# Performance work log

Hardware: AMD Instinct MI355X
Metric: run time of the kernel (lower is better)

Reference implementation:

```python
import jax, jax.numpy as jnp
from jax import lax
import numpy as np

C = 12        # input channels
H = 233       # lstm hidden
L = 6         # lstm layers
P = 96        # sliding window length
F = 96        # forecast steps
B = 16        # batch (treated as SEQ axis by the LSTM, matching the torch code)


def setup_inputs() -> dict:
    key = jax.random.key(0)
    ks = jax.random.split(key, 9)
    s = 1.0 / np.sqrt(H)  # pytorch default uniform init scale
    u = lambda k, shape: jax.random.uniform(k, shape, jnp.float32, -s, s)
    return {
        "X": jax.random.normal(ks[0], (B, P, C), jnp.float32),
        "Wih0": u(ks[1], (4 * H, C)),        # layer 0 input weights
        "Wih": u(ks[2], (L - 1, 4 * H, H)),  # layers 1..5 input weights
        "Whh": u(ks[3], (L, 4 * H, H)),
        "bih": u(ks[4], (L, 4 * H)),
        "bhh": u(ks[5], (L, 4 * H)),
        "Wl": u(ks[6], (C, H)),
        "bl": u(ks[7], (C,)),
    }


def _lstm_layer(x, wih, whh, b):
    # x: (S, N, in) -> (S, N, H); scan over seq axis 0, gate order i,f,g,o (pytorch)
    N = x.shape[1]
    h0 = jnp.zeros((N, H), x.dtype)

    def cell(carry, xt):
        h, c = carry
        gates = xt @ wih.T + h @ whh.T + b          # (N, 4H)
        i, f, g, o = jnp.split(gates, 4, axis=-1)
        c = jax.nn.sigmoid(f) * c + jax.nn.sigmoid(i) * jnp.tanh(g)
        h = jax.nn.sigmoid(o) * jnp.tanh(c)
        return (h, c), h

    _, ys = lax.scan(cell, (h0, h0), x)
    return ys


def reference(X, Wih0, Wih, Whh, bih, bhh, Wl, bl):
    # Faithful to torch: nn.LSTM without batch_first treats axis0=B as seq,
    # axis1=P as batch; output[0][:, -1, :] picks the last window position.
    def step(window, _):
        x = _lstm_layer(window, Wih0, Whh[0], bih[0] + bhh[0])
        for l in range(1, L):
            x = _lstm_layer(x, Wih[l - 1], Whh[l], bih[l] + bhh[l])
        h_last = x[:, -1, :]              # (B, H)
        new = h_last @ Wl.T + bl          # (B, C)
        window = jnp.concatenate([window[:, 1:, :], new[:, None, :]], axis=1)
        return window, new

    _, toks = lax.scan(step, X, None, length=F)   # (F, B, C)
    return jnp.transpose(toks, (1, 0, 2))          # (B, F, C)
```

## Files before the change

### kernel.cpp

```cpp
#include <hip/hip_runtime.h>

#define HND    233
#define NL     6
#define GPL    8
#define UPW    32
#define ROWS   128
#define TSTEPS 16
#define FSTEPS 96
#define NSLOT  (TSTEPS*FSTEPS)
#define CDIM   12
#define G4H    (4*HND)
#define HP     240
#define VINW   496
#define NTICK  (6*95+15+1)
#define NHEAD  3
#define BLOCK  512
#define NWORD  234
#define AG     __HIP_MEMORY_SCOPE_AGENT
#define SENT   0x7FBADBADu
#define PLIM   (1L << 18)

typedef unsigned long long u64;

__device__ __forceinline__ float sigf(float x) { return 1.f / (1.f + expf(-x)); }
__device__ __forceinline__ bool rdy(u64 v) {
  return ((unsigned)v != SENT) && ((unsigned)(v >> 32) != SENT);
}

__device__ __forceinline__ int build(int m, int* fl, int* tl) {
  const int fh0 = m / 6;
  const int f_hi = (fh0 > 95) ? 95 : fh0;
  const int f_lo = (m < 10) ? 0 : (m - 10) / 6;
  const int ns = f_hi - f_lo + 1;
  #pragma unroll
  for (int k = 0; k < 3; ++k) { fl[k] = f_lo + k; tl[k] = m - 6 * (f_lo + k); }
  return ns;
}

__global__ void init_kernel(unsigned* __restrict__ hout, int hp) {
  size_t i = (size_t)blockIdx.x * blockDim.x + threadIdx.x;
  size_t stride = (size_t)gridDim.x * blockDim.x;
  const size_t nh = (size_t)NL * NSLOT * hp;
  for (size_t k = i; k < nh; k += stride) hout[k] = ((int)(k % hp) < HND) ? SENT : 0u;
}

__global__ void __launch_bounds__(BLOCK, 1) lstm_pipe(
    const float* __restrict__ X,
    const float* __restrict__ Wih0, const float* __restrict__ Wih,
    const float* __restrict__ Whh,  const float* __restrict__ bih,
    const float* __restrict__ bhh,  const float* __restrict__ Wl,
    const float* __restrict__ bl,   float* __restrict__ out,
    float* __restrict__ hout, int hps) {
  __shared__ float vin[3][VINW];
  __shared__ float bias[ROWS];
  __shared__ float foldb[ROWS];
  __shared__ float cst[3][UPW];
  __shared__ float wih0s[ROWS][CDIM];
  __shared__ float xs[TSTEPS][CDIM];
  __shared__ float wlh[CDIM][HP];

  const int tid = threadIdx.x;
  const int bid = blockIdx.x;
  u64* hu = (u64*)hout;

  if (bid >= NL * GPL) {
    const int hid = bid - NL * GPL;
    for (int i = tid; i < CDIM * HP; i += BLOCK) {
      int rr = i / HP, k = i % HP;
      ((float*)wlh)[i] = (k < HND) ? Wl[rr * HND + k] : 0.f;
    }
    for (int i = tid; i < VINW; i += BLOCK) vin[0][i] = 0.f;
    __syncthreads();
    for (int f = hid; f < FSTEPS; f += NHEAD) {
      for (int t = 0; t < TSTEPS; ++t) {
        if (tid < 117) {
          const u64* src = hu + ((size_t)5 * NSLOT + 16 * f + t) * hps + tid;
          u64 v; long gd = 0;
          for (;;) {
            v = __hip_atomic_load(src, __ATOMIC_RELAXED, AG);
            if (rdy(v)) break;
            if (++gd > PLIM) break;
            if (gd > 4) __builtin_amdgcn_s_sleep(1);
          }
          *(u64*)&vin[0][2 * tid] = v;
        }
        __syncthreads();
        if (tid < 48) {
          int rr = tid >> 2, q = tid & 3;
          const float4* wr = (const float4*)&wlh[rr][0];
          const float4* hv = (const float4*)&vin[0][0];
          float a = 0.f;
          #pragma unroll
          for (int c = 0; c < 15; ++c) {
            float4 x0 = wr[q * 15 + c], y0 = hv[q * 15 + c];
            a = fmaf(x0.w, y0.w, fmaf(x0.z, y0.z, fmaf(x0.y, y0.y, fmaf(x0.x, y0.x, a))));
          }
          a += __shfl_xor(a, 1);
          a += __shfl_xor(a, 2);
          if (q == 0) out[((size_t)t * FSTEPS + f) * CDIM + rr] = a + bl[rr];
        }
        __syncthreads();
      }
    }
    return;
  }

  const int l = bid / GPL, g = bid % GPL;
  const int j0 = g * UPW;
  const int U = min(UPW, HND - j0);
  const int wave = tid >> 6, ln = tid & 63;
  const int rr = ln & 15, q = ln >> 4;
  const int row = wave * 16 + rr;
  const int u = row >> 2, gt = row & 3;
  const int grow = gt * HND + j0 + u;
  const bool rowok = (u < U);

  if (l == 0) {
    for (int i = tid; i < CDIM * HP; i += BLOCK) {
      int r2 = i / HP, k = i % HP;
      ((float*)wlh)[i] = (k < HND) ? Wl[r2 * HND + k] : 0.f;
    }
    for (int i = tid; i < ROWS * CDIM; i += BLOCK) {
      int r2 = i / CDIM, c = i % CDIM;
      int uu = r2 >> 2, g2 = r2 & 3;
      wih0s[r2][c] = (uu < U) ? Wih0[(g2 * HND + j0 + uu) * CDIM + c] : 0.f;
    }
    for (int i = tid; i < TSTEPS * CDIM; i += BLOCK)
      xs[i / CDIM][i % CDIM] = X[((size_t)(i / CDIM) * 96 + 95) * CDIM + (i % CDIM)];
  }
  for (int i = tid; i < 3 * VINW; i += BLOCK) ((float*)vin)[i] = 0.f;
  __syncthreads();

  float4 w4[30];
  const float* wihl = Wih + (size_t)(l - 1) * G4H * HND;
  const float* whhl = Whh + (size_t)l * G4H * HND;
  #pragma unroll
  for (int j = 0; j < 30; ++j) {
    float e[4];
    #pragma unroll
    for (int ee = 0; ee < 4; ++ee) {
      const int idx = (q * 30 + j) * 4 + ee;
      float v = 0.f;
      if (rowok) {
        if (idx < HND) {
          if (l == 0) {
            float acc = 0.f;
            #pragma unroll
            for (int c = 0; c < CDIM; ++c) acc = fmaf(wih0s[row][c], wlh[c][idx], acc);
            v = acc;
          } else {
            v = wihl[(size_t)grow * HND + idx];
          }
        } else if (idx >= HP && idx < HP + HND) {
          v = whhl[(size_t)grow * HND + (idx - HP)];
        }
      }
      e[ee] = v;
    }
    w4[j] = make_float4(e[0], e[1], e[2], e[3]);
  }
  if (tid < ROWS) {
    float b = 0.f, fb = 0.f;
    if ((tid >> 2) < U) {
      const int gr2 = (tid & 3) * HND + j0 + (tid >> 2);
      b = bih[l * G4H + gr2] + bhh[l * G4H + gr2];
      if (l == 0) {
        #pragma unroll
        for (int c = 0; c < CDIM; ++c) fb = fmaf(wih0s[tid][c], bl[c], fb);
      }
    }
    bias[tid] = b;
    foldb[tid] = fb;
  }
  __syncthreads();

  int fl[3], tl[3];

  for (int m = 0; m < NTICK; ++m) {
    const int ns = build(m, fl, tl);

    const u64 *s0 = nullptr, *s1 = nullptr;
    u64 *d0 = nullptr, *d1 = nullptr;

    auto setup = [&](int w, const u64*& sp, u64*& dp) {
      const int k = w / NWORD;
      if (k >= ns) return;
      const int f = fl[k], t = tl[k], sg = f % 3;
      const int o = w - k * NWORD;
      if (o < 117) {
        if (l == 0 && f == 0) return;
        sp = (l == 0)
           ? hu + ((size_t)5 * NSLOT + 16 * (f - 1) + t) * hps + o
           : hu + ((size_t)(l - 1) * NSLOT + 16 * f + t) * hps + o;
        dp = (u64*)&vin[sg][2 * o];
      } else {
        const int jj = o - 117;
        float* dst = &vin[sg][HP + 2 * jj];
        if (t == 0) { dst[0] = 0.f; dst[1] = 0.f; return; }
        if ((jj >> 4) == g) return;
        sp = hu + ((size_t)l * NSLOT + 16 * f + (t - 1)) * hps + jj;
        dp = (u64*)dst;
      }
    };
    setup(tid, s0, d0);
    if (tid + BLOCK < 3 * NWORD) setup(tid + BLOCK, s1, d1);

    long gd = 0;
    while (s0 || s1) {
      if (s0) { u64 v = __hip_atomic_load(s0, __ATOMIC_RELAXED, AG);
                if (rdy(v)) { *d0 = v; s0 = nullptr; } }
      if (s1) { u64 v = __hip_atomic_load(s1, __ATOMIC_RELAXED, AG);
                if (rdy(v)) { *d1 = v; s1 = nullptr; } }
      if (++gd > PLIM) break;
      if (gd > 6) __builtin_amdgcn_s_sleep(1);
    }
    __syncthreads();

    float r0 = 0.f, r1 = 0.f, r2 = 0.f;
    {
      const float4* va = (const float4*)&vin[fl[0] % 3][0];
      float a = 0.f;
      #pragma unroll
      for (int j = 0; j < 30; ++j) {
        const float4 wv = w4[j];
        const float4 y = va[q * 30 + j];
        a = fmaf(wv.x, y.x, fmaf(wv.y, y.y, fmaf(wv.z, y.z, fmaf(wv.w, y.w, a))));
      }
      a += __shfl_xor(a, 16);
      a += __shfl_xor(a, 32);
      r0 = a + bias[row];
    }
    if (ns > 1) {
      const float4* vb = (const float4*)&vin[fl[1] % 3][0];
      float a = 0.f;
      #pragma unroll
      for (int j = 0; j < 30; ++j) {
        const float4 wv = w4[j];
        const float4 y = vb[q * 30 + j];
        a = fmaf(wv.x, y.x, fmaf(wv.y, y.y, fmaf(wv.z, y.z, fmaf(wv.w, y.w, a))));
      }
      a += __shfl_xor(a, 16);
      a += __shfl_xor(a, 32);
      r1 = a + bias[row];
    }
    if (ns > 2) {
      const float4* vc = (const float4*)&vin[fl[2] % 3][0];
      float a = 0.f;
      #pragma unroll
      for (int j = 0; j < 30; ++j) {
        const float4 wv = w4[j];
        const float4 y = vc[q * 30 + j];
        a = fmaf(wv.x, y.x, fmaf(wv.y, y.y, fmaf(wv.z, y.z, fmaf(wv.w, y.w, a))));
      }
      a += __shfl_xor(a, 16);
      a += __shfl_xor(a, 32);
      r2 = a + bias[row];
    }
    __syncthreads();

    const int v4 = ln & 3;
    const int uu = 4 * wave + v4;
    const int rowc = 4 * uu;
    #pragma unroll
    for (int k = 0; k < 3; ++k) {
      if (k >= ns) break;
      const int f = fl[k], t = tl[k], b3 = f % 3;
      const float gv = (k == 0) ? r0 : (k == 1) ? r1 : r2;
      float hn = 0.f;
      float gg[4];
      #pragma unroll
      for (int g2 = 0; g2 < 4; ++g2) gg[g2] = __shfl(gv, 4 * v4 + g2);
      if (ln < 4 && uu < U) {
        #pragma unroll
        for (int g2 = 0; g2 < 4; ++g2) {
          if (l == 0) {
            if (f == 0) {
              float s = gg[g2];
              #pragma unroll
              for (int c = 0; c < CDIM; ++c) s = fmaf(wih0s[rowc + g2][c], xs[t][c], s);
              gg[g2] = s;
            } else {
              gg[g2] += foldb[rowc + g2];
            }
          }
        }
        const float cp = (t == 0) ? 0.f : cst[b3][uu];
        const float cn = sigf(gg[1]) * cp + sigf(gg[0]) * tanhf(gg[2]);
        hn = sigf(gg[3]) * tanhf(cn);
        cst[b3][uu] = cn;
        vin[b3][HP + j0 + uu] = hn;
      }
      const float lo = __shfl(hn, 2 * (ln & 1));
      const float hi = __shfl(hn, 2 * (ln & 1) + 1);
      if (ln < 2) {
        const int pairu = 4 * wave + 2 * ln;
        if (pairu < U) {
          const u64 pv = ((u64)__float_as_uint(hi) << 32) | (u64)__float_as_uint(lo);
          __hip_atomic_store(hu + ((size_t)l * NSLOT + 16 * f + t) * hps +
                                 (j0 >> 1) + (pairu >> 1),
                             pv, __ATOMIC_RELAXED, AG);
        }
      }
    }
  }
}

extern "C" void kernel_launch(void* const* d_in, const int* in_sizes, int n_in,
                              void* d_out, int out_size, void* d_ws, size_t ws_size,
                              hipStream_t stream) {
  const float* X    = (const float*)d_in[0];
  const float* Wih0 = (const float*)d_in[1];
  const float* Wih  = (const float*)d_in[2];
  const float* Whh  = (const float*)d_in[3];
  const float* bih  = (const float*)d_in[4];
  const float* bhh  = (const float*)d_in[5];
  const float* Wl   = (const float*)d_in[6];
  const float* bl   = (const float*)d_in[7];

  const size_t HN = (size_t)NL * NSLOT;
  const int hp = (ws_size >= HN * 240 * 4) ? 240 : 234;
  float* hout = (float*)d_ws;

  init_kernel<<<2048, 256, 0, stream>>>((unsigned*)hout, hp);
  lstm_pipe<<<NL * GPL + NHEAD, BLOCK, 0, stream>>>(
      X, Wih0, Wih, Whh, bih, bhh, Wl, bl, (float*)d_out, hout, hp / 2);
}
```

Measured before the change: 2.762 ms.

## Spread LSTM units over more blocks and double-buffer per-tick input vectors

Each layer now spans 15 blocks of 256 threads, 16 units each, instead of 8 blocks of 512 threads with 32 units. The per-tick input vectors are double-buffered by tick parity and slot index, which removes the second barrier between the matvec and the cell update. Cell state moves from shared memory into registers. The three matvecs are fused into one loop that reuses each weight load. This spreads the serial recurrent work over more CUs, but more blocks now poll the flags and more cross-block traffic is needed per tick.

```diff
diff --git a/kernel.cpp b/kernel.cpp
--- a/kernel.cpp
+++ b/kernel.cpp
@@ -2,19 +2,19 @@
 
 #define HND    233
 #define NL     6
-#define GPL    8
-#define UPW    32
-#define ROWS   128
+#define GPL    15
+#define UPW    16
+#define ROWS   64
 #define TSTEPS 16
 #define FSTEPS 96
 #define NSLOT  (TSTEPS*FSTEPS)
 #define CDIM   12
 #define G4H    (4*HND)
 #define HP     240
-#define VINW   496
+#define RL     480
 #define NTICK  (6*95+15+1)
 #define NHEAD  3
-#define BLOCK  512
+#define BLOCK  256
 #define NWORD  234
 #define AG     __HIP_MEMORY_SCOPE_AGENT
 #define SENT   0x7FBADBADu
@@ -31,10 +31,9 @@
   const int fh0 = m / 6;
   const int f_hi = (fh0 > 95) ? 95 : fh0;
   const int f_lo = (m < 10) ? 0 : (m - 10) / 6;
-  const int ns = f_hi - f_lo + 1;
   #pragma unroll
   for (int k = 0; k < 3; ++k) { fl[k] = f_lo + k; tl[k] = m - 6 * (f_lo + k); }
-  return ns;
+  return f_hi - f_lo + 1;
 }
 
 __global__ void init_kernel(unsigned* __restrict__ hout, int hp) {
@@ -51,10 +50,9 @@
     const float* __restrict__ bhh,  const float* __restrict__ Wl,
     const float* __restrict__ bl,   float* __restrict__ out,
     float* __restrict__ hout, int hps) {
-  __shared__ float vin[3][VINW];
+  __shared__ float vin[2][3][RL];
   __shared__ float bias[ROWS];
   __shared__ float foldb[ROWS];
-  __shared__ float cst[3][UPW];
   __shared__ float wih0s[ROWS][CDIM];
   __shared__ float xs[TSTEPS][CDIM];
   __shared__ float wlh[CDIM][HP];
@@ -69,7 +67,7 @@
       int rr = i / HP, k = i % HP;
       ((float*)wlh)[i] = (k < HND) ? Wl[rr * HND + k] : 0.f;
     }
-    for (int i = tid; i < VINW; i += BLOCK) vin[0][i] = 0.f;
+    for (int i = tid; i < RL; i += BLOCK) vin[0][0][i] = 0.f;
     __syncthreads();
     for (int f = hid; f < FSTEPS; f += NHEAD) {
       for (int t = 0; t < TSTEPS; ++t) {
@@ -82,13 +80,13 @@
             if (++gd > PLIM) break;
             if (gd > 4) __builtin_amdgcn_s_sleep(1);
           }
-          *(u64*)&vin[0][2 * tid] = v;
+          *(u64*)&vin[0][0][2 * tid] = v;
         }
         __syncthreads();
         if (tid < 48) {
           int rr = tid >> 2, q = tid & 3;
           const float4* wr = (const float4*)&wlh[rr][0];
-          const float4* hv = (const float4*)&vin[0][0];
+          const float4* hv = (const float4*)&vin[0][0][0];
           float a = 0.f;
           #pragma unroll
           for (int c = 0; c < 15; ++c) {
@@ -128,7 +126,7 @@
     for (int i = tid; i < TSTEPS * CDIM; i += BLOCK)
       xs[i / CDIM][i % CDIM] = X[((size_t)(i / CDIM) * 96 + 95) * CDIM + (i % CDIM)];
   }
-  for (int i = tid; i < 3 * VINW; i += BLOCK) ((float*)vin)[i] = 0.f;
+  for (int i = tid; i < 2 * 3 * RL; i += BLOCK) ((float*)vin)[i] = 0.f;
   __syncthreads();
 
   float4 w4[30];
@@ -174,132 +172,118 @@
   }
   __syncthreads();
 
+  float cs0 = 0.f, cs1 = 0.f, cs2 = 0.f;
+  const int v4 = ln & 3;
+  const int ug = j0 + 4 * wave + v4;
   int fl[3], tl[3];
 
   for (int m = 0; m < NTICK; ++m) {
     const int ns = build(m, fl, tl);
-
-    const u64 *s0 = nullptr, *s1 = nullptr;
-    u64 *d0 = nullptr, *d1 = nullptr;
+    const int p = m & 1;
+
+    const u64 *s0 = nullptr, *s1 = nullptr, *s2 = nullptr;
+    u64 *d0 = nullptr, *d1 = nullptr, *d2 = nullptr;
 
     auto setup = [&](int w, const u64*& sp, u64*& dp) {
       const int k = w / NWORD;
       if (k >= ns) return;
-      const int f = fl[k], t = tl[k], sg = f % 3;
+      const int f = fl[k], t = tl[k];
       const int o = w - k * NWORD;
       if (o < 117) {
-        if (l == 0 && f == 0) return;
+        float* dst = &vin[p][k][2 * o];
+        if (l == 0 && f == 0) { dst[0] = 0.f; dst[1] = 0.f; return; }
         sp = (l == 0)
            ? hu + ((size_t)5 * NSLOT + 16 * (f - 1) + t) * hps + o
            : hu + ((size_t)(l - 1) * NSLOT + 16 * f + t) * hps + o;
-        dp = (u64*)&vin[sg][2 * o];
+        dp = (u64*)dst;
       } else {
         const int jj = o - 117;
-        float* dst = &vin[sg][HP + 2 * jj];
+        float* dst = &vin[p][k][HP + 2 * jj];
         if (t == 0) { dst[0] = 0.f; dst[1] = 0.f; return; }
-        if ((jj >> 4) == g) return;
+        if ((jj >> 3) == g) return;
         sp = hu + ((size_t)l * NSLOT + 16 * f + (t - 1)) * hps + jj;
         dp = (u64*)dst;
       }
     };
     setup(tid, s0, d0);
-    if (tid + BLOCK < 3 * NWORD) setup(tid + BLOCK, s1, d1);
+    setup(tid + 256, s1, d1);
+    if (tid + 512 < 3 * NWORD) setup(tid + 512, s2, d2);
 
     long gd = 0;
-    while (s0 || s1) {
+    while (s0 || s1 || s2) {
       if (s0) { u64 v = __hip_atomic_load(s0, __ATOMIC_RELAXED, AG);
                 if (rdy(v)) { *d0 = v; s0 = nullptr; } }
       if (s1) { u64 v = __hip_atomic_load(s1, __ATOMIC_RELAXED, AG);
                 if (rdy(v)) { *d1 = v; s1 = nullptr; } }
+      if (s2) { u64 v = __hip_atomic_load(s2, __ATOMIC_RELAXED, AG);
+                if (rdy(v)) { *d2 = v; s2 = nullptr; } }
       if (++gd > PLIM) break;
-      if (gd > 6) __builtin_amdgcn_s_sleep(1);
+      if (gd > 8) __builtin_amdgcn_s_sleep(1);
     }
     __syncthreads();
 
-    float r0 = 0.f, r1 = 0.f, r2 = 0.f;
-    {
-      const float4* va = (const float4*)&vin[fl[0] % 3][0];
-      float a = 0.f;
-      #pragma unroll
-      for (int j = 0; j < 30; ++j) {
-        const float4 wv = w4[j];
-        const float4 y = va[q * 30 + j];
-        a = fmaf(wv.x, y.x, fmaf(wv.y, y.y, fmaf(wv.z, y.z, fmaf(wv.w, y.w, a))));
-      }
-      a += __shfl_xor(a, 16);
-      a += __shfl_xor(a, 32);
-      r0 = a + bias[row];
-    }
-    if (ns > 1) {
-      const float4* vb = (const float4*)&vin[fl[1] % 3][0];
-      float a = 0.f;
-      #pragma unroll
-      for (int j = 0; j < 30; ++j) {
-        const float4 wv = w4[j];
-        const float4 y = vb[q * 30 + j];
-        a = fmaf(wv.x, y.x, fmaf(wv.y, y.y, fmaf(wv.z, y.z, fmaf(wv.w, y.w, a))));
-      }
-      a += __shfl_xor(a, 16);
-      a += __shfl_xor(a, 32);
-      r1 = a + bias[row];
-    }
-    if (ns > 2) {
-      const float4* vc = (const float4*)&vin[fl[2] % 3][0];
-      float a = 0.f;
-      #pragma unroll
-      for (int j = 0; j < 30; ++j) {
-        const float4 wv = w4[j];
-        const float4 y = vc[q * 30 + j];
-        a = fmaf(wv.x, y.x, fmaf(wv.y, y.y, fmaf(wv.z, y.z, fmaf(wv.w, y.w, a))));
-      }
-      a += __shfl_xor(a, 16);
-      a += __shfl_xor(a, 32);
-      r2 = a + bias[row];
-    }
-    __syncthreads();
-
-    const int v4 = ln & 3;
-    const int uu = 4 * wave + v4;
-    const int rowc = 4 * uu;
+    const float4* va = (const float4*)&vin[p][0][0];
+    const float4* vb = (const float4*)&vin[p][1][0];
+    const float4* vc = (const float4*)&vin[p][2][0];
+    float a0 = 0.f, a1 = 0.f, a2 = 0.f;
+    #pragma unroll
+    for (int j = 0; j < 30; ++j) {
+      const int c = q * 30 + j;
+      const float4 wv = w4[j];
+      const float4 y0 = va[c];
+      const float4 y1 = vb[c];
+      const float4 y2 = vc[c];
+      a0 = fmaf(wv.x, y0.x, fmaf(wv.y, y0.y, fmaf(wv.z, y0.z, fmaf(wv.w, y0.w, a0))));
+      a1 = fmaf(wv.x, y1.x, fmaf(wv.y, y1.y, fmaf(wv.z, y1.z, fmaf(wv.w, y1.w, a1))));
+      a2 = fmaf(wv.x, y2.x, fmaf(wv.y, y2.y, fmaf(wv.z, y2.z, fmaf(wv.w, y2.w, a2))));
+    }
+    a0 += __shfl_xor(a0, 16); a0 += __shfl_xor(a0, 32);
+    a1 += __shfl_xor(a1, 16); a1 += __shfl_xor(a1, 32);
+    a2 += __shfl_xor(a2, 16); a2 += __shfl_xor(a2, 32);
+    const float bv = bias[row];
+    a0 += bv; a1 += bv; a2 += bv;
+
+    const int fl2next = ((m + 1) < 10) ? 0 : (m + 1 - 10) / 6;
     #pragma unroll
     for (int k = 0; k < 3; ++k) {
       if (k >= ns) break;
-      const int f = fl[k], t = tl[k], b3 = f % 3;
-      const float gv = (k == 0) ? r0 : (k == 1) ? r1 : r2;
-      float hn = 0.f;
+      const int f = fl[k], t = tl[k];
+      const int b3 = f % 3;
+      const float gv = (k == 0) ? a0 : (k == 1) ? a1 : a2;
       float gg[4];
       #pragma unroll
       for (int g2 = 0; g2 < 4; ++g2) gg[g2] = __shfl(gv, 4 * v4 + g2);
-      if (ln < 4 && uu < U) {
-        #pragma unroll
-        for (int g2 = 0; g2 < 4; ++g2) {
-          if (l == 0) {
-            if (f == 0) {
+      float hn = 0.f;
+      if (ln < 4 && ug < HND) {
+        const int rowc = 16 * wave + 4 * v4;
+        if (l == 0) {
+          if (f == 0) {
+            #pragma unroll
+            for (int g2 = 0; g2 < 4; ++g2) {
               float s = gg[g2];
               #pragma unroll
               for (int c = 0; c < CDIM; ++c) s = fmaf(wih0s[rowc + g2][c], xs[t][c], s);
               gg[g2] = s;
-            } else {
-              gg[g2] += foldb[rowc + g2];
             }
+          } else {
+            #pragma unroll
+            for (int g2 = 0; g2 < 4; ++g2) gg[g2] += foldb[rowc + g2];
           }
         }
-        const float cp = (t == 0) ? 0.f : cst[b3][uu];
+        const float cp = (t == 0) ? 0.f : (b3 == 0 ? cs0 : (b3 == 1 ? cs1 : cs2));
         const float cn = sigf(gg[1]) * cp + sigf(gg[0]) * tanhf(gg[2]);
         hn = sigf(gg[3]) * tanhf(cn);
-        cst[b3][uu] = cn;
-        vin[b3][HP + j0 + uu] = hn;
-      }
-      const float lo = __shfl(hn, 2 * (ln & 1));
-      const float hi = __shfl(hn, 2 * (ln & 1) + 1);
-      if (ln < 2) {
-        const int pairu = 4 * wave + 2 * ln;
-        if (pairu < U) {
-          const u64 pv = ((u64)__float_as_uint(hi) << 32) | (u64)__float_as_uint(lo);
-          __hip_atomic_store(hu + ((size_t)l * NSLOT + 16 * f + t) * hps +
-                                 (j0 >> 1) + (pairu >> 1),
-                             pv, __ATOMIC_RELAXED, AG);
-        }
+        if (b3 == 0) cs0 = cn; else if (b3 == 1) cs1 = cn; else cs2 = cn;
+        if (t < 15)
+          vin[p ^ 1][f - fl2next][HP + ug] = hn;
+      }
+      const float lo = __shfl(hn, 2 * ln);
+      const float hi = __shfl(hn, 2 * ln + 1);
+      const int pu = j0 + 4 * wave + 2 * ln;
+      if (ln < 2 && pu < HND) {
+        const u64 pv = ((u64)__float_as_uint(hi) << 32) | (u64)__float_as_uint(lo);
+        __hip_atomic_store(hu + ((size_t)l * NSLOT + 16 * f + t) * hps + (pu >> 1),
+                           pv, __ATOMIC_RELAXED, AG);
       }
     }
   }
```

Measured after the change: 2.592 ms. -6.1%, faster.

## Switch to per-block push mailboxes with 15 groups per layer

Applied to the files above, without the earlier changes.

Each layer now runs on 15 blocks of 256 threads, with 16 hidden units per block instead of 8 blocks of 512. The shared global h-output array is replaced by per-block mailbox buffers that producers push into directly. Consumers reset each slot to the sentinel after reading it, so a 16-slot ring can be reused. The gate dot-product partials now go through shared memory, and one set of lanes does the reduction and cell update before scattering packed h pairs to downstream and peer mailboxes. This is meant to spread the work over more CUs and make polling local. It costs many more remote atomic stores per step and relies on slot reuse being correctly ordered.

```diff
diff --git a/kernel.cpp b/kernel.cpp
--- a/kernel.cpp
+++ b/kernel.cpp
@@ -2,9 +2,9 @@
 
 #define HND    233
 #define NL     6
-#define GPL    8
-#define UPW    32
-#define ROWS   128
+#define GPL    15
+#define UPW    16
+#define ROWS   64
 #define TSTEPS 16
 #define FSTEPS 96
 #define NSLOT  (TSTEPS*FSTEPS)
@@ -14,10 +14,15 @@
 #define VINW   496
 #define NTICK  (6*95+15+1)
 #define NHEAD  3
-#define BLOCK  512
+#define BLOCK  256
 #define NWORD  234
+#define RLW    240
+#define MBC    (16*RLW)
+#define NMB    (NL*GPL)
+#define H5W    120
 #define AG     __HIP_MEMORY_SCOPE_AGENT
 #define SENT   0x7FBADBADu
+#define SENT64 0x7FBADBAD7FBADBADull
 #define PLIM   (1L << 18)
 
 typedef unsigned long long u64;
@@ -31,17 +36,15 @@
   const int fh0 = m / 6;
   const int f_hi = (fh0 > 95) ? 95 : fh0;
   const int f_lo = (m < 10) ? 0 : (m - 10) / 6;
-  const int ns = f_hi - f_lo + 1;
   #pragma unroll
   for (int k = 0; k < 3; ++k) { fl[k] = f_lo + k; tl[k] = m - 6 * (f_lo + k); }
-  return ns;
-}
-
-__global__ void init_kernel(unsigned* __restrict__ hout, int hp) {
+  return f_hi - f_lo + 1;
+}
+
+__global__ void init_kernel(u64* __restrict__ buf, size_t n) {
   size_t i = (size_t)blockIdx.x * blockDim.x + threadIdx.x;
-  size_t stride = (size_t)gridDim.x * blockDim.x;
-  const size_t nh = (size_t)NL * NSLOT * hp;
-  for (size_t k = i; k < nh; k += stride) hout[k] = ((int)(k % hp) < HND) ? SENT : 0u;
+  size_t st = (size_t)gridDim.x * blockDim.x;
+  for (size_t k = i; k < n; k += st) buf[k] = SENT64;
 }
 
 __global__ void __launch_bounds__(BLOCK, 1) lstm_pipe(
@@ -50,8 +53,9 @@
     const float* __restrict__ Whh,  const float* __restrict__ bih,
     const float* __restrict__ bhh,  const float* __restrict__ Wl,
     const float* __restrict__ bl,   float* __restrict__ out,
-    float* __restrict__ hout, int hps) {
+    u64* __restrict__ mbu, u64* __restrict__ h5u) {
   __shared__ float vin[3][VINW];
+  __shared__ float part[3][BLOCK];
   __shared__ float bias[ROWS];
   __shared__ float foldb[ROWS];
   __shared__ float cst[3][UPW];
@@ -61,7 +65,6 @@
 
   const int tid = threadIdx.x;
   const int bid = blockIdx.x;
-  u64* hu = (u64*)hout;
 
   if (bid >= NL * GPL) {
     const int hid = bid - NL * GPL;
@@ -74,7 +77,7 @@
     for (int f = hid; f < FSTEPS; f += NHEAD) {
       for (int t = 0; t < TSTEPS; ++t) {
         if (tid < 117) {
-          const u64* src = hu + ((size_t)5 * NSLOT + 16 * f + t) * hps + tid;
+          const u64* src = h5u + (size_t)(16 * f + t) * H5W + tid;
           u64 v; long gd = 0;
           for (;;) {
             v = __hip_atomic_load(src, __ATOMIC_RELAXED, AG);
@@ -108,12 +111,11 @@
   const int l = bid / GPL, g = bid % GPL;
   const int j0 = g * UPW;
   const int U = min(UPW, HND - j0);
-  const int wave = tid >> 6, ln = tid & 63;
-  const int rr = ln & 15, q = ln >> 4;
-  const int row = wave * 16 + rr;
-  const int u = row >> 2, gt = row & 3;
+  const int r = tid & 63, q = tid >> 6;
+  const int u = r >> 2, gt = r & 3;
   const int grow = gt * HND + j0 + u;
   const bool rowok = (u < U);
+  u64* mbOwn = mbu + (size_t)(l * GPL + g) * MBC;
 
   if (l == 0) {
     for (int i = tid; i < CDIM * HP; i += BLOCK) {
@@ -131,22 +133,22 @@
   for (int i = tid; i < 3 * VINW; i += BLOCK) ((float*)vin)[i] = 0.f;
   __syncthreads();
 
-  float4 w4[30];
+  float4 w4[31];
   const float* wihl = Wih + (size_t)(l - 1) * G4H * HND;
   const float* whhl = Whh + (size_t)l * G4H * HND;
   #pragma unroll
-  for (int j = 0; j < 30; ++j) {
+  for (int j = 0; j < 31; ++j) {
     float e[4];
     #pragma unroll
     for (int ee = 0; ee < 4; ++ee) {
-      const int idx = (q * 30 + j) * 4 + ee;
+      const int idx = (q * 31 + j) * 4 + ee;
       float v = 0.f;
       if (rowok) {
         if (idx < HND) {
           if (l == 0) {
             float acc = 0.f;
             #pragma unroll
-            for (int c = 0; c < CDIM; ++c) acc = fmaf(wih0s[row][c], wlh[c][idx], acc);
+            for (int c = 0; c < CDIM; ++c) acc = fmaf(wih0s[r][c], wlh[c][idx], acc);
             v = acc;
           } else {
             v = wihl[(size_t)grow * HND + idx];
@@ -179,127 +181,142 @@
   for (int m = 0; m < NTICK; ++m) {
     const int ns = build(m, fl, tl);
 
-    const u64 *s0 = nullptr, *s1 = nullptr;
-    u64 *d0 = nullptr, *d1 = nullptr;
-
-    auto setup = [&](int w, const u64*& sp, u64*& dp) {
+    u64 *s0 = nullptr, *s1 = nullptr, *s2 = nullptr;
+    u64 *d0 = nullptr, *d1 = nullptr, *d2 = nullptr;
+
+    auto setup = [&](int w, u64*& sp, u64*& dp) {
       const int k = w / NWORD;
       if (k >= ns) return;
-      const int f = fl[k], t = tl[k], sg = f % 3;
+      const int f = fl[k], t = tl[k];
       const int o = w - k * NWORD;
       if (o < 117) {
-        if (l == 0 && f == 0) return;
-        sp = (l == 0)
-           ? hu + ((size_t)5 * NSLOT + 16 * (f - 1) + t) * hps + o
-           : hu + ((size_t)(l - 1) * NSLOT + 16 * f + t) * hps + o;
-        dp = (u64*)&vin[sg][2 * o];
+        float* dst = &vin[k][2 * o];
+        if (l == 0 && f == 0) { dst[0] = 0.f; dst[1] = 0.f; return; }
+        sp = mbOwn + (size_t)t * RLW + o;
+        dp = (u64*)dst;
       } else {
         const int jj = o - 117;
-        float* dst = &vin[sg][HP + 2 * jj];
+        float* dst = &vin[k][HP + 2 * jj];
         if (t == 0) { dst[0] = 0.f; dst[1] = 0.f; return; }
-        if ((jj >> 4) == g) return;
-        sp = hu + ((size_t)l * NSLOT + 16 * f + (t - 1)) * hps + jj;
+        if ((jj >> 3) == g) return;
+        sp = mbOwn + (size_t)(t - 1) * RLW + 117 + jj;
         dp = (u64*)dst;
       }
     };
     setup(tid, s0, d0);
-    if (tid + BLOCK < 3 * NWORD) setup(tid + BLOCK, s1, d1);
+    setup(tid + 256, s1, d1);
+    if (tid + 512 < 3 * NWORD) setup(tid + 512, s2, d2);
+    u64 *q0 = s0, *q1 = s1, *q2 = s2;
 
     long gd = 0;
-    while (s0 || s1) {
+    while (s0 || s1 || s2) {
       if (s0) { u64 v = __hip_atomic_load(s0, __ATOMIC_RELAXED, AG);
                 if (rdy(v)) { *d0 = v; s0 = nullptr; } }
       if (s1) { u64 v = __hip_atomic_load(s1, __ATOMIC_RELAXED, AG);
                 if (rdy(v)) { *d1 = v; s1 = nullptr; } }
+      if (s2) { u64 v = __hip_atomic_load(s2, __ATOMIC_RELAXED, AG);
+                if (rdy(v)) { *d2 = v; s2 = nullptr; } }
       if (++gd > PLIM) break;
-      if (gd > 6) __builtin_amdgcn_s_sleep(1);
-    }
+      if (gd > 8) __builtin_amdgcn_s_sleep(1);
+    }
+    if (q0) __hip_atomic_store(q0, SENT64, __ATOMIC_RELAXED, AG);
+    if (q1) __hip_atomic_store(q1, SENT64, __ATOMIC_RELAXED, AG);
+    if (q2) __hip_atomic_store(q2, SENT64, __ATOMIC_RELAXED, AG);
     __syncthreads();
 
-    float r0 = 0.f, r1 = 0.f, r2 = 0.f;
     {
-      const float4* va = (const float4*)&vin[fl[0] % 3][0];
+      const float4* va = (const float4*)&vin[0][0];
       float a = 0.f;
       #pragma unroll
-      for (int j = 0; j < 30; ++j) {
+      for (int j = 0; j < 31; ++j) {
         const float4 wv = w4[j];
-        const float4 y = va[q * 30 + j];
+        const float4 y = va[q * 31 + j];
         a = fmaf(wv.x, y.x, fmaf(wv.y, y.y, fmaf(wv.z, y.z, fmaf(wv.w, y.w, a))));
       }
-      a += __shfl_xor(a, 16);
-      a += __shfl_xor(a, 32);
-      r0 = a + bias[row];
+      part[0][tid] = a;
     }
     if (ns > 1) {
-      const float4* vb = (const float4*)&vin[fl[1] % 3][0];
+      const float4* vb = (const float4*)&vin[1][0];
       float a = 0.f;
       #pragma unroll
-      for (int j = 0; j < 30; ++j) {
+      for (int j = 0; j < 31; ++j) {
         const float4 wv = w4[j];
-        const float4 y = vb[q * 30 + j];
+        const float4 y = vb[q * 31 + j];
         a = fmaf(wv.x, y.x, fmaf(wv.y, y.y, fmaf(wv.z, y.z, fmaf(wv.w, y.w, a))));
       }
-      a += __shfl_xor(a, 16);
-      a += __shfl_xor(a, 32);
-      r1 = a + bias[row];
+      part[1][tid] = a;
     }
     if (ns > 2) {
-      const float4* vc = (const float4*)&vin[fl[2] % 3][0];
+      const float4* vc = (const float4*)&vin[2][0];
       float a = 0.f;
       #pragma unroll
-      for (int j = 0; j < 30; ++j) {
+      for (int j = 0; j < 31; ++j) {
         const float4 wv = w4[j];
-        const float4 y = vc[q * 30 + j];
+        const float4 y = vc[q * 31 + j];
         a = fmaf(wv.x, y.x, fmaf(wv.y, y.y, fmaf(wv.z, y.z, fmaf(wv.w, y.w, a))));
       }
-      a += __shfl_xor(a, 16);
-      a += __shfl_xor(a, 32);
-      r2 = a + bias[row];
+      part[2][tid] = a;
     }
     __syncthreads();
 
-    const int v4 = ln & 3;
-    const int uu = 4 * wave + v4;
-    const int rowc = 4 * uu;
-    #pragma unroll
-    for (int k = 0; k < 3; ++k) {
-      if (k >= ns) break;
-      const int f = fl[k], t = tl[k], b3 = f % 3;
-      const float gv = (k == 0) ? r0 : (k == 1) ? r1 : r2;
-      float hn = 0.f;
+    float hn = 0.f;
+    const int kc = tid >> 4, uu = tid & 15;
+    if (tid < 48 && kc < ns) {
+      const int f = fl[kc], t = tl[kc], b3 = f % 3;
       float gg[4];
       #pragma unroll
-      for (int g2 = 0; g2 < 4; ++g2) gg[g2] = __shfl(gv, 4 * v4 + g2);
-      if (ln < 4 && uu < U) {
-        #pragma unroll
-        for (int g2 = 0; g2 < 4; ++g2) {
-          if (l == 0) {
-            if (f == 0) {
-              float s = gg[g2];
-              #pragma unroll
-              for (int c = 0; c < CDIM; ++c) s = fmaf(wih0s[rowc + g2][c], xs[t][c], s);
-              gg[g2] = s;
-            } else {
-              gg[g2] += foldb[rowc + g2];
-            }
+      for (int g2 = 0; g2 < 4; ++g2) {
+        const int rr = 4 * uu + g2;
+        float s = part[kc][rr] + part[kc][rr + 64] + part[kc][rr + 128] +
+                  part[kc][rr + 192] + bias[rr];
+        if (l == 0) {
+          if (f == 0) {
+            #pragma unroll
+            for (int c = 0; c < CDIM; ++c) s = fmaf(wih0s[rr][c], xs[t][c], s);
+          } else {
+            s += foldb[rr];
           }
         }
+        gg[g2] = s;
+      }
+      if (uu < U) {
         const float cp = (t == 0) ? 0.f : cst[b3][uu];
         const float cn = sigf(gg[1]) * cp + sigf(gg[0]) * tanhf(gg[2]);
         hn = sigf(gg[3]) * tanhf(cn);
         cst[b3][uu] = cn;
-        vin[b3][HP + j0 + uu] = hn;
-      }
-      const float lo = __shfl(hn, 2 * (ln & 1));
-      const float hi = __shfl(hn, 2 * (ln & 1) + 1);
-      if (ln < 2) {
-        const int pairu = 4 * wave + 2 * ln;
-        if (pairu < U) {
-          const u64 pv = ((u64)__float_as_uint(hi) << 32) | (u64)__float_as_uint(lo);
-          __hip_atomic_store(hu + ((size_t)l * NSLOT + 16 * f + t) * hps +
-                                 (j0 >> 1) + (pairu >> 1),
-                             pv, __ATOMIC_RELAXED, AG);
-        }
+        if (t < 15) {
+          const int fln = ((m + 1) < 10) ? 0 : (m + 1 - 10) / 6;
+          vin[f - fln][HP + j0 + uu] = hn;
+        }
+      }
+    }
+
+    if (tid < 64) {
+      #pragma unroll
+      for (int base = 0; base < 768; base += 64) {
+        const int idx = base + tid;
+        const int k = idx / 240;
+        const int rem = idx - k * 240;
+        const int d = rem >> 3, j = rem & 7;
+        const float lo = __shfl(hn, 16 * k + 2 * j);
+        const float hi = __shfl(hn, 16 * k + 2 * j + 1);
+        if (idx >= 720 || k >= ns) continue;
+        const int pu = j0 + 2 * j;
+        if (pu >= HND) continue;
+        const int f = fl[k], t = tl[k];
+        const u64 pv = ((u64)__float_as_uint(hi) << 32) | (u64)__float_as_uint(lo);
+        u64* dst;
+        if (d < 15) {
+          const int lup = (l == 5) ? 0 : (l + 1);
+          dst = mbu + (size_t)(lup * GPL + d) * MBC + (size_t)t * RLW + (j0 >> 1) + j;
+        } else if (d < 29) {
+          int dd = d - 15; dd += (dd >= g);
+          dst = mbu + (size_t)(l * GPL + dd) * MBC + (size_t)t * RLW + 117 + (j0 >> 1) + j;
+        } else {
+          if (l != 5) continue;
+          dst = h5u + (size_t)(16 * f + t) * H5W + (j0 >> 1) + j;
+        }
+        __hip_atomic_store(dst, pv, __ATOMIC_RELAXED, AG);
       }
     }
   }
@@ -317,11 +334,11 @@
   const float* Wl   = (const float*)d_in[6];
   const float* bl   = (const float*)d_in[7];
 
-  const size_t HN = (size_t)NL * NSLOT;
-  const int hp = (ws_size >= HN * 240 * 4) ? 240 : 234;
-  float* hout = (float*)d_ws;
-
-  init_kernel<<<2048, 256, 0, stream>>>((unsigned*)hout, hp);
+  u64* mbu = (u64*)d_ws;
+  u64* h5u = mbu + (size_t)NMB * MBC;
+  const size_t nwords = (size_t)NMB * MBC + (size_t)NSLOT * H5W;
+
+  init_kernel<<<1024, 256, 0, stream>>>(mbu, nwords);
   lstm_pipe<<<NL * GPL + NHEAD, BLOCK, 0, stream>>>(
-      X, Wih0, Wih, Whh, bih, bhh, Wl, bl, (float*)d_out, hout, hp / 2);
-}
+      X, Wih0, Wih, Whh, bih, bhh, Wl, bl, (float*)d_out, mbu, h5u);
+}
```

After: 4.969 ms. 79.9% more time.
